# Kernel tuning notes

Hardware: AMD Instinct MI355X
Metric: run time of the kernel (lower is better)

The kernel has to match this reference:

```python
import jax, jax.numpy as jnp
import numpy as np

WINDOW = 512
RATIO = 4
NEG = float(jnp.finfo(jnp.bfloat16).min)


def _topk_idxs(S: int, window: int, ratio: int):
    # window indices: for row i, last `window` causal positions, -1 where invalid
    base = jnp.arange(S)[:, None]                      # [S,1]
    w = min(S, window)
    win = jnp.clip(base - window + 1, 0) + jnp.arange(w)  # [S,w]
    win = jnp.where(win > base, -1, win)
    # compressed-KV indices: row i sees first (i+1)//ratio compressed tokens, offset by S
    Sc = S // ratio
    mat = jnp.broadcast_to(jnp.arange(Sc), (S, Sc))    # [S,Sc]
    cmask = mat >= (jnp.arange(1, S + 1)[:, None] // ratio)
    comp = jnp.where(cmask, -1, mat + S)
    return jnp.concatenate([win, comp], axis=-1)       # [S, w+Sc]


def setup_inputs() -> dict:
    key = jax.random.key(0)
    k1, k2, k3, k4 = jax.random.split(key, 4)
    B, S, H, D = 1, 2048, 16, 128
    return {
        "query_states": jax.random.normal(k1, (B, S, H, D), jnp.float32),
        "kv_states": jax.random.normal(k2, (B, S, D), jnp.float32),
        "attn_sink": jax.random.normal(k3, (H,), jnp.float32),
        "kv_compress": jax.random.normal(k4, (B, S // RATIO, D), jnp.float32),
    }


def reference(query_states, kv_states, attn_sink, kv_compress):
    B, S, H, D = query_states.shape
    scale = D ** -0.5
    kv = jnp.concatenate([kv_states, kv_compress], axis=1)  # [B, KV, D]
    KV = kv.shape[1]
    q = jnp.transpose(query_states, (0, 2, 1, 3))            # [B, H, S, D]
    attn = jnp.einsum('bhsd,bkd->bhsk', q, kv) * scale       # [B, H, S, KV]
    # additive mask from topk indices; -1 wraps to padding column KV, then trimmed
    idxs = _topk_idxs(S, WINDOW, RATIO)                       # [S, K]
    mask = jnp.full((S, KV + 1), NEG, dtype=attn.dtype)
    mask = mask.at[jnp.arange(S)[:, None], idxs].set(0.0)[:, :-1]  # [S, KV]
    attn = attn + mask[None, None]
    sinks = jnp.broadcast_to(attn_sink.reshape(1, H, 1, 1), (B, H, S, 1))
    logits = jnp.concatenate([attn, sinks], axis=-1)          # [B, H, S, KV+1]
    probs = jax.nn.softmax(logits, axis=-1)
    scores = probs[..., :-1]
    out = jnp.einsum('bhsk,bkd->bhsd', scores, kv)
    return jnp.transpose(out, (0, 2, 1, 3))                   # [B, S, H, D]
```

## Files before the change

kernel.cpp:

```cpp
#include <hip/hip_runtime.h>


typedef __attribute__((ext_vector_type(8))) short bf16x8;
typedef __attribute__((ext_vector_type(4))) float f32x4;
typedef unsigned short u16;
typedef unsigned int u32;

constexpr int S = 2048, H = 16, D = 128, WIN = 512;
constexpr int QB = 4, HG = 8;
constexpr int NT = 256;

__device__ __forceinline__ u16 f2bf(float f) {
  u32 u = __builtin_bit_cast(u32, f);
  return (u16)((u + 0x7FFFu + ((u >> 16) & 1u)) >> 16);
}

__global__ __launch_bounds__(NT, 3) void sparse_attn_mfma2(
    const float* __restrict__ q, const float* __restrict__ kvs,
    const float* __restrict__ sink, const float* __restrict__ kvc,
    float* __restrict__ out) {

  const int it = (int)(gridDim.x - 1u - blockIdx.x);
  const int i0 = it * QB;
  const int h0 = blockIdx.y * HG;
  const int tid = threadIdx.x;
  const int wave = tid >> 6, lane = tid & 63;
  const int split = wave >> 1, mtg = wave & 1;
  const int lm = lane & 15, lg = lane >> 4;

  __shared__ __align__(16) char smem[41984];
  u16 (*Ksub)[8][4][16] = (u16(*)[8][4][16])(smem + split * 8192);
  u16 (*KTl)[40]        = (u16(*)[40])(smem + 16384 + split * 10240);
  u16 (*Pll)[40]        = (u16(*)[40])(smem + 36864 + wave * 1280);

  const int iq = i0 + (lm & 3);
  const int hh = h0 + mtg * 4 + (lm >> 2);

  const float qscale = 0.08838834764831845f;
  bf16x8 qf[4];
  {
    const float* qp = q + ((size_t)iq * H + hh) * D;
#pragma unroll
    for (int kt = 0; kt < 4; ++kt) {
      const float4* p4 = (const float4*)(qp + kt * 32 + lg * 8);
      float4 a = p4[0], b = p4[1];
      bf16x8 v;
      v[0] = (short)f2bf(a.x * qscale); v[1] = (short)f2bf(a.y * qscale);
      v[2] = (short)f2bf(a.z * qscale); v[3] = (short)f2bf(a.w * qscale);
      v[4] = (short)f2bf(b.x * qscale); v[5] = (short)f2bf(b.y * qscale);
      v[6] = (short)f2bf(b.z * qscale); v[7] = (short)f2bf(b.w * qscale);
      qf[kt] = v;
    }
  }

  const float sk = sink[hh];
  float m_run = sk, l_run = 0.f;
  f32x4 oacc[8];
  const f32x4 fzero = {0.f, 0.f, 0.f, 0.f};
#pragma unroll
  for (int b = 0; b < 8; ++b) oacc[b] = fzero;

  const int w_lo = (i0 > WIN - 1) ? (i0 - (WIN - 1)) : 0;
  const int n1r = i0 + QB - w_lo;
  const int n2r = (i0 + QB) >> 2;
  const int nt1 = (n1r + 31) >> 5;
  const int nt2 = (n2r + 31) >> 5;
  const int ntiles = nt1 + nt2;
  const int kmax = (ntiles + 1) >> 1;

  const int st = tid & 127;
  const int st_t7 = st & 7, st_r0 = st_t7 * 4, st_dc = st >> 3;

  float4 sreg[8];
  auto sload = [&](int tt) {
    const float* src; int row0, nv;
    if (tt < nt1) { src = kvs; row0 = w_lo + tt * 32; nv = n1r - tt * 32; }
    else          { src = kvc; row0 = (tt - nt1) * 32; nv = n2r - (tt - nt1) * 32; }
    if (nv > 32) nv = 32;
    const float* p = src + (size_t)(row0 + st_r0) * D + st_dc * 8;
#pragma unroll
    for (int rr = 0; rr < 4; ++rr) {
      bool ok = (st_r0 + rr) < nv;
      const float4* p4 = (const float4*)(p + (size_t)rr * D);
      sreg[rr * 2 + 0] = ok ? p4[0] : make_float4(0.f, 0.f, 0.f, 0.f);
      sreg[rr * 2 + 1] = ok ? p4[1] : make_float4(0.f, 0.f, 0.f, 0.f);
    }
  };

  auto swrite = [&]() {
    u16 bfv[4][8];
#pragma unroll
    for (int rr = 0; rr < 4; ++rr) {
      const float4& x = sreg[rr * 2];
      const float4& y = sreg[rr * 2 + 1];
      bfv[rr][0] = f2bf(x.x); bfv[rr][1] = f2bf(x.y);
      bfv[rr][2] = f2bf(x.z); bfv[rr][3] = f2bf(x.w);
      bfv[rr][4] = f2bf(y.x); bfv[rr][5] = f2bf(y.y);
      bfv[rr][6] = f2bf(y.z); bfv[rr][7] = f2bf(y.w);
    }
#pragma unroll
    for (int rr = 0; rr < 4; ++rr) {
      int rowp = rr ^ (st_t7 & 3);
      bf16x8 v;
#pragma unroll
      for (int e = 0; e < 8; ++e) v[e] = (short)bfv[rr][e];
      *(bf16x8*)&Ksub[st_t7][st_dc >> 1][rowp][(st_dc & 1) * 8] = v;
    }
#pragma unroll
    for (int dd = 0; dd < 8; ++dd) {
      int dl = st_dc * 8 + dd;
      int dphys = (dl & ~7) | (dd ^ (st_dc & 7));
      uint2 w2 = make_uint2((u32)bfv[0][dd] | ((u32)bfv[1][dd] << 16),
                            (u32)bfv[2][dd] | ((u32)bfv[3][dd] << 16));
      *(uint2*)&KTl[dphys][st_r0] = w2;
    }
  };

  sload(split);

  const int rrA = (lm & 3) ^ ((lm >> 2) & 3);

  for (int k = 0; k < kmax; ++k) {
    const int tt = 2 * k + split;
    const bool active = tt < ntiles;
    __syncthreads();
    if (active) swrite();
    __syncthreads();
    const int tn = tt + 2;
    if (tn < ntiles) sload(tn);
    if (!active) continue;

    const bool isw = tt < nt1;
    const int row0 = isw ? (w_lo + tt * 32) : ((tt - nt1) * 32);

    f32x4 tacc[2];
    tacc[0] = fzero; tacc[1] = fzero;
#pragma unroll
    for (int kt = 0; kt < 4; ++kt) {
      const int ds = kt * 2 + (lg >> 1), co = (lg & 1) * 8;
      bf16x8 a0 = *(const bf16x8*)&Ksub[(lm >> 2)][ds][rrA][co];
      bf16x8 a1 = *(const bf16x8*)&Ksub[4 + (lm >> 2)][ds][rrA][co];
      tacc[0] = __builtin_amdgcn_mfma_f32_16x16x32_bf16(a0, qf[kt], tacc[0], 0, 0, 0);
      tacc[1] = __builtin_amdgcn_mfma_f32_16x16x32_bf16(a1, qf[kt], tacc[1], 0, 0, 0);
    }

    float vv[8];
    float tm = -1e30f;
#pragma unroll
    for (int k2 = 0; k2 < 2; ++k2) {
#pragma unroll
      for (int r = 0; r < 4; ++r) {
        int jj = row0 + k2 * 16 + lg * 4 + r;
        float x = tacc[k2][r];
        bool ok = isw ? (jj <= iq && jj + WIN > iq) : (jj * 4 + 3 <= iq);
        x = ok ? x : -1e30f;
        vv[k2 * 4 + r] = x;
        tm = fmaxf(tm, x);
      }
    }
    tm = fmaxf(tm, __shfl_xor(tm, 16));
    tm = fmaxf(tm, __shfl_xor(tm, 32));
    if (__any(tm > m_run + 8.f)) {
      float mn = fmaxf(m_run, tm);
      float fs = __expf(m_run - mn);
      m_run = mn; l_run *= fs;
#pragma unroll
      for (int dt = 0; dt < 8; ++dt) oacc[dt] *= fs;
    }
    float s = 0.f;
#pragma unroll
    for (int k2 = 0; k2 < 2; ++k2) {
      u16 pb[4];
#pragma unroll
      for (int r = 0; r < 4; ++r) {
        float p = __expf(vv[k2 * 4 + r] - m_run);
        s += p; pb[r] = f2bf(p);
      }
      *(uint2*)&Pll[lm][k2 * 16 + lg * 4] =
          make_uint2((u32)pb[0] | ((u32)pb[1] << 16),
                     (u32)pb[2] | ((u32)pb[3] << 16));
    }
    l_run += s;

    bf16x8 pf = *(const bf16x8*)&Pll[lm][lg * 8];
#pragma unroll
    for (int dt = 0; dt < 8; ++dt) {
      int d = dt * 16 + lm;
      int drow = (d & ~7) | ((d & 7) ^ ((d >> 3) & 7));
      bf16x8 vf = *(const bf16x8*)&KTl[drow][lg * 8];
      oacc[dt] = __builtin_amdgcn_mfma_f32_16x16x32_bf16(vf, pf, oacc[dt], 0, 0, 0);
    }
  }

  float l = l_run;
  l += __shfl_xor(l, 16);
  l += __shfl_xor(l, 32);

  float (*Ocomb)[16][128] = (float(*)[16][128])(smem);
  float* Mcomb = (float*)(smem + 16384);
  float* Lcomb = (float*)(smem + 16384 + 128);

  __syncthreads();
  if (split == 1) {
#pragma unroll
    for (int dt = 0; dt < 8; ++dt)
      *(f32x4*)&Ocomb[mtg][lm][dt * 16 + lg * 4] = oacc[dt];
    if (lg == 0) { Mcomb[mtg * 16 + lm] = m_run; Lcomb[mtg * 16 + lm] = l; }
  }
  __syncthreads();
  if (split == 0) {
    float m1 = Mcomb[mtg * 16 + lm], l1 = Lcomb[mtg * 16 + lm];
    float mf = fmaxf(m_run, m1);
    float a0 = __expf(m_run - mf), a1 = __expf(m1 - mf);
    float lf = l * a0 + l1 * a1 + __expf(sk - mf);
    float di = 1.f / lf;
    float* op = out + ((size_t)iq * H + hh) * D;
#pragma unroll
    for (int dt = 0; dt < 8; ++dt) {
      f32x4 o1 = *(f32x4*)&Ocomb[mtg][lm][dt * 16 + lg * 4];
      float4 w4 = make_float4((oacc[dt][0] * a0 + o1[0] * a1) * di,
                              (oacc[dt][1] * a0 + o1[1] * a1) * di,
                              (oacc[dt][2] * a0 + o1[2] * a1) * di,
                              (oacc[dt][3] * a0 + o1[3] * a1) * di);
      *(float4*)(op + dt * 16 + lg * 4) = w4;
    }
  }
}

extern "C" void kernel_launch(void* const* d_in, const int* in_sizes, int n_in,
                              void* d_out, int out_size, void* d_ws, size_t ws_size,
                              hipStream_t stream) {
  const float* q    = (const float*)d_in[0];
  const float* kvs  = (const float*)d_in[1];
  const float* sink = (const float*)d_in[2];
  const float* kvc  = (const float*)d_in[3];
  float* out = (float*)d_out;
  dim3 grid(S / QB, H / HG);
  sparse_attn_mfma2<<<grid, NT, 0, stream>>>(q, kvs, sink, kvc, out);
}
```

Measured before the change: 138.0 us.

## Pre-convert KV to bf16 in a prepass kernel and streamline tile staging

A new prepass kernel converts kv_states and kv_compress to one zero-padded bf16 buffer in workspace. The attention kernel then loads bf16 directly, which halves global traffic per tile and drops the per-tile conversion and bounds checks. The transposed LDS write now uses byte-permute instructions. The change also adds s_setprio around the MFMA blocks and a mask-free path for tiles that are fully valid. The cost is an extra kernel launch and a full pass over KV, and correctness depends on d_ws being large enough.

```diff
diff --git a/kernel.cpp b/kernel.cpp
--- a/kernel.cpp
+++ b/kernel.cpp
@@ -9,16 +9,38 @@
 constexpr int S = 2048, H = 16, D = 128, WIN = 512;
 constexpr int QB = 4, HG = 8;
 constexpr int NT = 256;
+constexpr int KVROWS = 2592;
 
 __device__ __forceinline__ u16 f2bf(float f) {
   u32 u = __builtin_bit_cast(u32, f);
   return (u16)((u + 0x7FFFu + ((u >> 16) & 1u)) >> 16);
 }
 
-__global__ __launch_bounds__(NT, 3) void sparse_attn_mfma2(
-    const float* __restrict__ q, const float* __restrict__ kvs,
-    const float* __restrict__ sink, const float* __restrict__ kvc,
-    float* __restrict__ out) {
+__global__ __launch_bounds__(256) void precvt_kv(
+    const float* __restrict__ kvs, const float* __restrict__ kvc,
+    u16* __restrict__ dst) {
+  int idx = blockIdx.x * 256 + threadIdx.x;
+  if (idx >= KVROWS * (D / 8)) return;
+  int row = idx >> 4, c8 = (idx & 15) * 8;
+  float4 a = make_float4(0.f, 0.f, 0.f, 0.f), b = a;
+  if (row < 2048) {
+    const float4* p = (const float4*)(kvs + (size_t)row * D + c8);
+    a = p[0]; b = p[1];
+  } else if (row < 2560) {
+    const float4* p = (const float4*)(kvc + (size_t)(row - 2048) * D + c8);
+    a = p[0]; b = p[1];
+  }
+  bf16x8 v;
+  v[0] = (short)f2bf(a.x); v[1] = (short)f2bf(a.y);
+  v[2] = (short)f2bf(a.z); v[3] = (short)f2bf(a.w);
+  v[4] = (short)f2bf(b.x); v[5] = (short)f2bf(b.y);
+  v[6] = (short)f2bf(b.z); v[7] = (short)f2bf(b.w);
+  *(bf16x8*)(dst + (size_t)row * D + c8) = v;
+}
+
+__global__ __launch_bounds__(NT, 3) void sparse_attn_mfma3(
+    const float* __restrict__ q, const u16* __restrict__ kvb,
+    const float* __restrict__ sink, float* __restrict__ out) {
 
   const int it = (int)(gridDim.x - 1u - blockIdx.x);
   const int i0 = it * QB;
@@ -71,48 +93,36 @@
   const int st = tid & 127;
   const int st_t7 = st & 7, st_r0 = st_t7 * 4, st_dc = st >> 3;
 
-  float4 sreg[8];
+  uint4 sreg[4];
   auto sload = [&](int tt) {
-    const float* src; int row0, nv;
-    if (tt < nt1) { src = kvs; row0 = w_lo + tt * 32; nv = n1r - tt * 32; }
-    else          { src = kvc; row0 = (tt - nt1) * 32; nv = n2r - (tt - nt1) * 32; }
-    if (nv > 32) nv = 32;
-    const float* p = src + (size_t)(row0 + st_r0) * D + st_dc * 8;
-#pragma unroll
-    for (int rr = 0; rr < 4; ++rr) {
-      bool ok = (st_r0 + rr) < nv;
-      const float4* p4 = (const float4*)(p + (size_t)rr * D);
-      sreg[rr * 2 + 0] = ok ? p4[0] : make_float4(0.f, 0.f, 0.f, 0.f);
-      sreg[rr * 2 + 1] = ok ? p4[1] : make_float4(0.f, 0.f, 0.f, 0.f);
-    }
+    const int row0 = (tt < nt1) ? (w_lo + tt * 32) : (2048 + (tt - nt1) * 32);
+    const u16* p = kvb + (size_t)(row0 + st_r0) * D + st_dc * 8;
+#pragma unroll
+    for (int rr = 0; rr < 4; ++rr)
+      sreg[rr] = *(const uint4*)(p + (size_t)rr * D);
   };
 
   auto swrite = [&]() {
-    u16 bfv[4][8];
-#pragma unroll
-    for (int rr = 0; rr < 4; ++rr) {
-      const float4& x = sreg[rr * 2];
-      const float4& y = sreg[rr * 2 + 1];
-      bfv[rr][0] = f2bf(x.x); bfv[rr][1] = f2bf(x.y);
-      bfv[rr][2] = f2bf(x.z); bfv[rr][3] = f2bf(x.w);
-      bfv[rr][4] = f2bf(y.x); bfv[rr][5] = f2bf(y.y);
-      bfv[rr][6] = f2bf(y.z); bfv[rr][7] = f2bf(y.w);
-    }
 #pragma unroll
     for (int rr = 0; rr < 4; ++rr) {
       int rowp = rr ^ (st_t7 & 3);
-      bf16x8 v;
-#pragma unroll
-      for (int e = 0; e < 8; ++e) v[e] = (short)bfv[rr][e];
-      *(bf16x8*)&Ksub[st_t7][st_dc >> 1][rowp][(st_dc & 1) * 8] = v;
-    }
-#pragma unroll
-    for (int dd = 0; dd < 8; ++dd) {
-      int dl = st_dc * 8 + dd;
-      int dphys = (dl & ~7) | (dd ^ (st_dc & 7));
-      uint2 w2 = make_uint2((u32)bfv[0][dd] | ((u32)bfv[1][dd] << 16),
-                            (u32)bfv[2][dd] | ((u32)bfv[3][dd] << 16));
-      *(uint2*)&KTl[dphys][st_r0] = w2;
+      *(uint4*)&Ksub[st_t7][st_dc >> 1][rowp][(st_dc & 1) * 8] = sreg[rr];
+    }
+    const u32* R0 = (const u32*)&sreg[0];
+    const u32* R1 = (const u32*)&sreg[1];
+    const u32* R2 = (const u32*)&sreg[2];
+    const u32* R3 = (const u32*)&sreg[3];
+#pragma unroll
+    for (int dd2 = 0; dd2 < 4; ++dd2) {
+#pragma unroll
+      for (int h = 0; h < 2; ++h) {
+        const u32 sel = h ? 0x07060302u : 0x05040100u;
+        u32 lo = __builtin_amdgcn_perm(R1[dd2], R0[dd2], sel);
+        u32 hi = __builtin_amdgcn_perm(R3[dd2], R2[dd2], sel);
+        int dl = st_dc * 8 + dd2 * 2 + h;
+        int dphys = (dl & ~7) | ((dl & 7) ^ (st_dc & 7));
+        *(uint2*)&KTl[dphys][st_r0] = make_uint2(lo, hi);
+      }
     }
   };
 
@@ -135,6 +145,7 @@
 
     f32x4 tacc[2];
     tacc[0] = fzero; tacc[1] = fzero;
+    __builtin_amdgcn_s_setprio(1);
 #pragma unroll
     for (int kt = 0; kt < 4; ++kt) {
       const int ds = kt * 2 + (lg >> 1), co = (lg & 1) * 8;
@@ -143,20 +154,33 @@
       tacc[0] = __builtin_amdgcn_mfma_f32_16x16x32_bf16(a0, qf[kt], tacc[0], 0, 0, 0);
       tacc[1] = __builtin_amdgcn_mfma_f32_16x16x32_bf16(a1, qf[kt], tacc[1], 0, 0, 0);
     }
+    __builtin_amdgcn_s_setprio(0);
 
     float vv[8];
     float tm = -1e30f;
-#pragma unroll
-    for (int k2 = 0; k2 < 2; ++k2) {
-#pragma unroll
-      for (int r = 0; r < 4; ++r) {
-        int jj = row0 + k2 * 16 + lg * 4 + r;
-        float x = tacc[k2][r];
-        bool ok = isw ? (jj <= iq && jj + WIN > iq) : (jj * 4 + 3 <= iq);
-        x = ok ? x : -1e30f;
-        vv[k2 * 4 + r] = x;
-        tm = fmaxf(tm, x);
-      }
+    const bool fullv = isw ? (row0 >= i0 + 3 - (WIN - 1)) && (row0 + 31 <= i0)
+                           : ((row0 + 31) * 4 + 3 <= i0);
+    if (fullv) {
+#pragma unroll
+      for (int k2 = 0; k2 < 2; ++k2)
+#pragma unroll
+        for (int r = 0; r < 4; ++r) {
+          float x = tacc[k2][r];
+          vv[k2 * 4 + r] = x;
+          tm = fmaxf(tm, x);
+        }
+    } else {
+#pragma unroll
+      for (int k2 = 0; k2 < 2; ++k2)
+#pragma unroll
+        for (int r = 0; r < 4; ++r) {
+          int jj = row0 + k2 * 16 + lg * 4 + r;
+          float x = tacc[k2][r];
+          bool ok = isw ? (jj <= iq && jj + WIN > iq) : (jj * 4 + 3 <= iq);
+          x = ok ? x : -1e30f;
+          vv[k2 * 4 + r] = x;
+          tm = fmaxf(tm, x);
+        }
     }
     tm = fmaxf(tm, __shfl_xor(tm, 16));
     tm = fmaxf(tm, __shfl_xor(tm, 32));
@@ -183,6 +207,7 @@
     l_run += s;
 
     bf16x8 pf = *(const bf16x8*)&Pll[lm][lg * 8];
+    __builtin_amdgcn_s_setprio(1);
 #pragma unroll
     for (int dt = 0; dt < 8; ++dt) {
       int d = dt * 16 + lm;
@@ -190,6 +215,7 @@
       bf16x8 vf = *(const bf16x8*)&KTl[drow][lg * 8];
       oacc[dt] = __builtin_amdgcn_mfma_f32_16x16x32_bf16(vf, pf, oacc[dt], 0, 0, 0);
     }
+    __builtin_amdgcn_s_setprio(0);
   }
 
   float l = l_run;
@@ -235,6 +261,12 @@
   const float* sink = (const float*)d_in[2];
   const float* kvc  = (const float*)d_in[3];
   float* out = (float*)d_out;
+  u16* kvb = (u16*)d_ws;
+
+  {
+    int nthr = KVROWS * (D / 8);
+    precvt_kv<<<(nthr + 255) / 256, 256, 0, stream>>>(kvs, kvc, kvb);
+  }
   dim3 grid(S / QB, H / HG);
-  sparse_attn_mfma2<<<grid, NT, 0, stream>>>(q, kvs, sink, kvc, out);
-}
+  sparse_attn_mfma3<<<grid, NT, 0, stream>>>(q, kvb, sink, out);
+}
```

Measured after the change: 117.1 us. 1.18x faster.
